# Kernel tuning notes

Hardware: AMD Instinct MI355X
Metric: run time of the kernel (lower is better)

The kernel has to match this reference:

```python
import jax, jax.numpy as jnp
import numpy as np

N = 8000      # nodes
E = 64000     # edges
F = 2560      # in_channels
H = 8         # heads
C = 320       # out_channels per head
G = 16        # graphs in batch
SLOPE = 0.2   # GATv2 default negative_slope


def setup_inputs() -> dict:
    key = jax.random.key(0)
    ks = jax.random.split(key, 20)
    inp = {
        'x': jax.random.normal(ks[0], (N, F), jnp.float32),
        'edge_index': jax.random.randint(ks[1], (2, E), 0, N, dtype=jnp.int64),
        'edge_attr': jax.random.normal(ks[2], (E, 1), jnp.float32),
        'batch': jnp.sort(jax.random.randint(ks[3], (N,), 0, G, dtype=jnp.int64)),
    }
    s_in = 1.0 / np.sqrt(F).astype(np.float32)
    s_att = 1.0 / np.sqrt(C).astype(np.float32)
    k = 4
    for layer in (1, 2):
        inp[f'Wl{layer}'] = jax.random.normal(ks[k + 0], (F, H * C), jnp.float32) * s_in
        inp[f'bl{layer}'] = jnp.zeros((H * C,), jnp.float32)
        inp[f'Wr{layer}'] = jax.random.normal(ks[k + 1], (F, H * C), jnp.float32) * s_in
        inp[f'br{layer}'] = jnp.zeros((H * C,), jnp.float32)
        inp[f'We{layer}'] = jax.random.normal(ks[k + 2], (1, H * C), jnp.float32)
        inp[f'att{layer}'] = jax.random.normal(ks[k + 3], (H, C), jnp.float32) * s_att
        inp[f'bias{layer}'] = jnp.zeros((H * C,), jnp.float32)
        k += 4
    return inp


def gatv2_layer(x, src, dst, edge_attr, Wl, bl, Wr, br, We, att, bias):
    # x: [N,F] -> out: [N, H*C]
    xl = (x @ Wl + bl).reshape(N, H, C)   # source transform (aggregated)
    xr = (x @ Wr + br).reshape(N, H, C)   # target transform
    ee = (edge_attr @ We).reshape(E, H, C)
    m = jax.nn.leaky_relu(xl[src] + xr[dst] + ee, SLOPE)  # [E,H,C]
    score = jnp.einsum('ehc,hc->eh', m, att)               # [E,H]
    # segment softmax over incoming edges of each target node
    smax = jax.ops.segment_max(score, dst, num_segments=N)  # [N,H]
    ex = jnp.exp(score - smax[dst])
    denom = jax.ops.segment_sum(ex, dst, num_segments=N)    # [N,H]
    alpha = ex / denom[dst]                                  # [E,H]
    out = jax.ops.segment_sum(xl[src] * alpha[:, :, None], dst, num_segments=N)
    return out.reshape(N, H * C) + bias


def reference(x, edge_index, edge_attr, batch,
              Wl1, bl1, Wr1, br1, We1, att1, bias1,
              Wl2, bl2, Wr2, br2, We2, att2, bias2):
    src, dst = edge_index[0], edge_index[1]
    h = gatv2_layer(x, src, dst, edge_attr, Wl1, bl1, Wr1, br1, We1, att1, bias1)
    # dropout is identity in eval mode
    h = gatv2_layer(h, src, dst, edge_attr, Wl2, bl2, Wr2, br2, We2, att2, bias2)
    # global mean pool over graphs
    sums = jax.ops.segment_sum(h, batch, num_segments=G)                 # [G, H*C]
    cnt = jax.ops.segment_sum(jnp.ones((N, 1), h.dtype), batch, num_segments=G)
    return sums / jnp.maximum(cnt, 1.0)
```

## Files before the change

kernel.cpp:

```cpp
#include <hip/hip_runtime.h>

typedef unsigned short u16;
typedef _Float16 f16;
typedef _Float16 f16x8 __attribute__((ext_vector_type(8)));
typedef _Float16 f16x2 __attribute__((ext_vector_type(2)));
typedef float f32x4 __attribute__((ext_vector_type(4)));

#define AS1 __attribute__((address_space(1)))
#define AS3 __attribute__((address_space(3)))

constexpr int N_NODES = 8000;
constexpr int N_EDGES = 64000;
constexpr int F_IN    = 2560;
constexpr int HEADS   = 8;
constexpr int CPH     = 320;
constexpr int HC      = 2560;
constexpr int NW      = 5120;
constexpr int NGRAPH  = 16;
constexpr float SLOPE = 0.2f;

__global__ __launch_bounds__(256)
void cvt_f32_f16(const float* __restrict__ in, f16* __restrict__ out, int n)
{
  const int i = (blockIdx.x * 256 + threadIdx.x) * 4;
  if (i >= n) return;
  const float4 v = *(const float4*)(in + i);
  f16 o[4] = {(f16)v.x, (f16)v.y, (f16)v.z, (f16)v.w};
  *(ushort4*)(out + i) = *(const ushort4*)o;
}

__global__ __launch_bounds__(256)
void transpose_w(const float* __restrict__ in, f16* __restrict__ out)
{
  __shared__ u16 tile[64][66];
  const int bx = blockIdx.x * 64;
  const int by = blockIdx.y * 64;
  const int tx = threadIdx.x & 63;
  const int ty = threadIdx.x >> 6;
  #pragma unroll
  for (int i = ty; i < 64; i += 4) {
    f16 h = (f16)in[(size_t)(by + i) * HC + bx + tx];
    u16 u; __builtin_memcpy(&u, &h, 2);
    tile[i][tx] = u;
  }
  __syncthreads();
  #pragma unroll
  for (int i = ty; i < 64; i += 4) {
    u16 u = tile[tx][i];
    f16 h; __builtin_memcpy(&h, &u, 2);
    out[(size_t)(bx + i) * F_IN + by + tx] = h;
  }
}

__global__ __launch_bounds__(512, 2)
void gemm_fused(const f16* __restrict__ A, const f16* __restrict__ BT,
                const float* __restrict__ bl, const float* __restrict__ br,
                f16* __restrict__ XL, f16* __restrict__ XR)
{
  __shared__ __align__(16) f16 sm[65536];
  f16* const sA0 = sm;
  f16* const sA1 = sm + 16384;
  f16* const sB0 = sm + 32768;
  f16* const sB1 = sm + 49152;

  const int t    = threadIdx.x;
  const int lane = t & 63;
  const int wave = t >> 6;

  const int bid0 = (int)blockIdx.x;
  const int xcd  = bid0 & 7;
  const int ic   = bid0 >> 3;
  const int m0   = (xcd * 4 + (ic & 3)) * 256;
  const int n0   = (ic >> 2) * 256;

  const int fm = (wave >> 2) * 128;
  const int fn = (wave & 3) * 64;
  const int ml = lane & 15;
  const int lq = lane >> 4;

  auto stageA = [&](f16* D, int half, int kt) {
    const int k0 = kt * 64;
    #pragma unroll
    for (int jj = 0; jj < 2; ++jj) {
      const int s  = jj * 512 + t;
      const int r  = s >> 3;
      const int lc = (s & 7) ^ (r & 7);
      int gr = m0 + half * 128 + r;
      gr = (gr < N_NODES) ? gr : (N_NODES - 1);
      const f16* g = A + (size_t)gr * F_IN + k0 + lc * 8;
      __builtin_amdgcn_global_load_lds((AS1 const void*)g,
                                       (AS3 void*)(D + half * 8192 + s * 8), 16, 0, 0);
    }
  };
  auto stageB = [&](f16* D, int half, int kt) {
    const int k0 = kt * 64;
    #pragma unroll
    for (int jj = 0; jj < 2; ++jj) {
      const int s  = jj * 512 + t;
      const int r  = s >> 3;
      const int lc = (s & 7) ^ (r & 7);
      const f16* g = BT + (size_t)(n0 + half * 128 + r) * F_IN + k0 + lc * 8;
      __builtin_amdgcn_global_load_lds((AS1 const void*)g,
                                       (AS3 void*)(D + half * 8192 + s * 8), 16, 0, 0);
    }
  };
  auto ldA = [&](const f16* S, int i, int kk) -> f16x8 {
    const int row = fm + i * 16 + ml;
    const int p   = (kk * 4 + lq) ^ (row & 7);
    return *(const f16x8*)(S + row * 64 + p * 8);
  };
  auto ldB = [&](const f16* S, int j, int kk) -> f16x8 {
    const int row = fn + j * 16 + ml;
    const int p   = (kk * 4 + lq) ^ (row & 7);
    return *(const f16x8*)(S + row * 64 + p * 8);
  };

  f32x4 acc[8][4] = {};
  f16x8 bf[4][2];

#define MMROW(i, A0_, A1_)                                                                   \
    _Pragma("unroll")                                                                        \
    for (int j = 0; j < 4; ++j) {                                                            \
      acc[i][j] = __builtin_amdgcn_mfma_f32_16x16x32_f16(A0_, bf[j][0], acc[i][j], 0, 0, 0); \
      acc[i][j] = __builtin_amdgcn_mfma_f32_16x16x32_f16(A1_, bf[j][1], acc[i][j], 0, 0, 0); \
    }

#define PHASE(SA, q, STG)                          \
  {                                                \
    const f16x8 p00 = ldA(SA, 2*(q),     0);       \
    const f16x8 p01 = ldA(SA, 2*(q),     1);       \
    const f16x8 p10 = ldA(SA, 2*(q) + 1, 0);       \
    const f16x8 p11 = ldA(SA, 2*(q) + 1, 1);       \
    STG;                                           \
    __builtin_amdgcn_s_barrier();                  \
    __builtin_amdgcn_sched_barrier(0);             \
    __builtin_amdgcn_s_setprio(1);                 \
    MMROW(2*(q),     p00, p01)                     \
    MMROW(2*(q) + 1, p10, p11)                     \
    __builtin_amdgcn_s_setprio(0);                 \
  }

#define ENDPH() { __builtin_amdgcn_s_barrier(); __builtin_amdgcn_sched_barrier(0); }
#define LOADB(SB) { _Pragma("unroll") for (int j = 0; j < 4; ++j) { bf[j][0] = ldB(SB, j, 0); bf[j][1] = ldB(SB, j, 1); } }

  stageA(sA0, 0, 0); stageA(sA0, 1, 0);
  stageB(sB0, 0, 0); stageB(sB0, 1, 0);
  stageB(sB1, 0, 1); stageB(sB1, 1, 1);
  asm volatile("s_waitcnt vmcnt(4)" ::: "memory");
  __builtin_amdgcn_s_barrier();
  __builtin_amdgcn_sched_barrier(0);

  for (int it = 0; it < 20; ++it) {
    const int T  = 2 * it;
    const int t1 = T + 1;
    const int t2 = (T + 2 < 40) ? T + 2 : 39;
    const int t3 = (T + 3 < 40) ? T + 3 : 39;

    LOADB(sB0)
    PHASE(sA0, 0, stageA(sA1, 0, t1)) ENDPH()
    PHASE(sA0, 1, stageA(sA1, 1, t1)) ENDPH()
    PHASE(sA0, 2, stageB(sB0, 0, t2)) ENDPH()
    PHASE(sA0, 3, stageB(sB0, 1, t2))
    asm volatile("s_waitcnt vmcnt(4)" ::: "memory");
    ENDPH()
    LOADB(sB1)
    PHASE(sA1, 0, stageA(sA0, 0, t2)) ENDPH()
    PHASE(sA1, 1, stageA(sA0, 1, t2)) ENDPH()
    PHASE(sA1, 2, stageB(sB1, 0, t3)) ENDPH()
    PHASE(sA1, 3, stageB(sB1, 1, t3))
    asm volatile("s_waitcnt vmcnt(4)" ::: "memory");
    ENDPH()
  }

#undef MMROW
#undef PHASE
#undef ENDPH
#undef LOADB

  asm volatile("s_waitcnt vmcnt(0)" ::: "memory");
  __builtin_amdgcn_s_barrier();

  const bool left = (n0 < HC);
  f16* __restrict__ OUT = left ? XL : XR;
  const float* __restrict__ bias = left ? bl : br;
  const int nb = left ? n0 : (n0 - HC);
  const int rg = (lane >> 4) * 4;
  f16* const wbase = sm + wave * 8192;

  #pragma unroll
  for (int j = 0; j < 4; ++j) {
    const float bv = bias[nb + fn + j * 16 + ml];
    #pragma unroll
    for (int i = 0; i < 8; ++i) {
      #pragma unroll
      for (int r = 0; r < 4; ++r) {
        const int row = i * 16 + rg + r;
        const int col = j * 16 + ml;
        const int pc  = (col >> 3) ^ (row & 7);
        wbase[row * 64 + pc * 8 + (col & 7)] = (f16)(acc[i][j][r] + bv);
      }
    }
  }
  __syncthreads();
  #pragma unroll
  for (int it = 0; it < 16; ++it) {
    const int row = it * 8 + (lane >> 3);
    const int ch  = lane & 7;
    const int pc  = ch ^ (row & 7);
    const f16x8 v = *(const f16x8*)(wbase + row * 64 + pc * 8);
    const int gm = m0 + fm + row;
    if (gm < N_NODES)
      *(f16x8*)(OUT + (size_t)gm * HC + nb + fn + ch * 8) = v;
  }
}

__global__ __launch_bounds__(256)
void count_edges(const int* __restrict__ dst, int* __restrict__ counts)
{
  const int e = blockIdx.x * 256 + threadIdx.x;
  if (e < N_EDGES) atomicAdd(&counts[dst[e]], 1);
}

__global__ __launch_bounds__(256)
void scan_offsets(const int* __restrict__ counts, int* __restrict__ offs, int* __restrict__ cur)
{
  __shared__ int wtot[4];
  const int t = threadIdx.x;
  const int lane = t & 63, wave = t >> 6;
  const int base = t * 32;
  int loc[32];
  int run = 0;
  #pragma unroll
  for (int i = 0; i < 32; ++i) {
    const int idx = base + i;
    const int v = (idx < N_NODES) ? counts[idx] : 0;
    loc[i] = run;
    run += v;
  }
  int incl = run;
  #pragma unroll
  for (int off = 1; off < 64; off <<= 1) {
    int y = __shfl_up(incl, off, 64);
    if (lane >= off) incl += y;
  }
  const int excl = incl - run;
  if (lane == 63) wtot[wave] = incl;
  __syncthreads();
  int wb = 0;
  for (int wv = 0; wv < wave; ++wv) wb += wtot[wv];
  const int mybase = wb + excl;
  #pragma unroll
  for (int i = 0; i < 32; ++i) {
    const int idx = base + i;
    if (idx < N_NODES) { offs[idx] = mybase + loc[i]; cur[idx] = mybase + loc[i]; }
  }
  if (t == 255) offs[N_NODES] = wb + incl;
}

__global__ __launch_bounds__(256)
void fill_csr(const int* __restrict__ dst, int* __restrict__ cur, int* __restrict__ eids)
{
  const int e = blockIdx.x * 256 + threadIdx.x;
  if (e < N_EDGES) {
    const int p = atomicAdd(&cur[dst[e]], 1);
    eids[p] = e;
  }
}

__global__ __launch_bounds__(256)
void gat_edge_fused(const f16* __restrict__ XL, const f16* __restrict__ XR,
                    const float* __restrict__ We, const float* __restrict__ att,
                    const float* __restrict__ eattr,
                    const int* __restrict__ src,
                    const int* __restrict__ offs, const int* __restrict__ eids,
                    const float* __restrict__ bias,
                    f16* __restrict__ out)
{
  const int n    = blockIdx.x;
  const int t    = threadIdx.x;
  const int wave = t >> 6;
  const int lane = t & 63;
  const int half = lane >> 5;
  const int l32  = lane & 31;
  const int h    = wave * 2 + half;
  const int c8   = h * CPH + l32 * 8;
  const int c2   = h * CPH + 256 + l32 * 2;

  float xr[10], wv[10], av[10];
  {
    const f16x8 v8 = *(const f16x8*)(XR + (size_t)n * HC + c8);
    const f16x2 v2 = *(const f16x2*)(XR + (size_t)n * HC + c2);
    #pragma unroll
    for (int k = 0; k < 8; ++k) xr[k] = (float)v8[k];
    xr[8] = (float)v2[0]; xr[9] = (float)v2[1];
  }
  {
    const float4 w0 = *(const float4*)(We + c8);
    const float4 w1 = *(const float4*)(We + c8 + 4);
    const float4 a0 = *(const float4*)(att + c8);
    const float4 a1 = *(const float4*)(att + c8 + 4);
    wv[0]=w0.x; wv[1]=w0.y; wv[2]=w0.z; wv[3]=w0.w;
    wv[4]=w1.x; wv[5]=w1.y; wv[6]=w1.z; wv[7]=w1.w;
    av[0]=a0.x; av[1]=a0.y; av[2]=a0.z; av[3]=a0.w;
    av[4]=a1.x; av[5]=a1.y; av[6]=a1.z; av[7]=a1.w;
    wv[8] = We[c2]; wv[9] = We[c2 + 1];
    av[8] = att[c2]; av[9] = att[c2 + 1];
  }

  float m = -3.0e38f, l = 0.f;
  float acc[10];
  #pragma unroll
  for (int k = 0; k < 10; ++k) acc[k] = 0.f;

  const int b = offs[n], e = offs[n + 1];
  if (b < e) {
    int eidA = eids[b];
    int sA   = src[eidA];
    float eaA = eattr[eidA];
    f16x8 v8A = *(const f16x8*)(XL + (size_t)sA * HC + c8);
    f16x2 v2A = *(const f16x2*)(XL + (size_t)sA * HC + c2);
    int sB; float eaB;
    if (b + 1 < e) { const int eid = eids[b + 1]; sB = src[eid]; eaB = eattr[eid]; }
    else           { sB = sA; eaB = 0.f; }

    for (int p = b; p < e; ++p) {
      const f16* rowN = XL + (size_t)sB * HC;
      const f16x8 v8N = *(const f16x8*)(rowN + c8);
      const f16x2 v2N = *(const f16x2*)(rowN + c2);
      const int pn   = (p + 2 < e) ? (p + 2) : (e - 1);
      const int eidN = eids[pn];
      const int sC   = src[eidN];
      const float eaC = eattr[eidN];

      float xl[10];
      #pragma unroll
      for (int k = 0; k < 8; ++k) xl[k] = (float)v8A[k];
      xl[8] = (float)v2A[0]; xl[9] = (float)v2A[1];
      float partial = 0.f;
      #pragma unroll
      for (int k = 0; k < 10; ++k) {
        float v = xl[k] + xr[k] + eaA * wv[k];
        v = (v > 0.f) ? v : SLOPE * v;
        partial += v * av[k];
      }
      #pragma unroll
      for (int msk = 16; msk >= 1; msk >>= 1)
        partial += __shfl_xor(partial, msk, 64);
      const float sc    = partial;
      const float mn    = fmaxf(m, sc);
      const float scale = __expf(m - mn);
      const float w     = __expf(sc - mn);
      l = l * scale + w;
      #pragma unroll
      for (int k = 0; k < 10; ++k) acc[k] = acc[k] * scale + w * xl[k];
      m = mn;

      v8A = v8N; v2A = v2N; eaA = eaB;
      sB = sC; eaB = eaC;
    }
  }

  const float inv = (l > 0.f) ? 1.f / l : 0.f;
  f16x8 s8;
  #pragma unroll
  for (int k = 0; k < 8; ++k) s8[k] = (f16)(acc[k] * inv + bias[c8 + k]);
  f16x2 s2;
  s2[0] = (f16)(acc[8] * inv + bias[c2]);
  s2[1] = (f16)(acc[9] * inv + bias[c2 + 1]);
  *(f16x8*)(out + (size_t)n * HC + c8) = s8;
  *(f16x2*)(out + (size_t)n * HC + c2) = s2;
}

__global__ __launch_bounds__(256)
void pool_kernel(const f16* __restrict__ Hm, const int* __restrict__ batch, float* __restrict__ out)
{
  __shared__ int se[2];
  const int g = blockIdx.x;
  const int chunk = blockIdx.y;
  const int t = threadIdx.x;
  if (t < 2) {
    const int target = g + t;
    int lo = 0, hi = N_NODES;
    while (lo < hi) { const int mid = (lo + hi) >> 1; if (batch[mid] < target) lo = mid + 1; else hi = mid; }
    se[t] = lo;
  }
  __syncthreads();
  const int s0 = se[0], s1 = se[1];
  const int c = chunk * 256 + t;
  float sum = 0.f;
  for (int n = s0; n < s1; ++n) sum += (float)Hm[(size_t)n * HC + c];
  int cnt = s1 - s0; if (cnt < 1) cnt = 1;
  out[g * HC + c] = sum / (float)cnt;
}

static void run_layer(const f16* A, const float* Wl, const float* bl,
                      const float* Wr, const float* br,
                      const float* We, const float* att, const float* bias,
                      const int* src, const float* eattr,
                      f16* WT, f16* XL, f16* XR,
                      const int* offs, const int* eids, f16* OUT, hipStream_t stream)
{
  dim3 tgrid(HC / 64, F_IN / 64);
  transpose_w<<<tgrid, 256, 0, stream>>>(Wl, WT);
  transpose_w<<<tgrid, 256, 0, stream>>>(Wr, WT + (size_t)HC * F_IN);
  gemm_fused<<<32 * (NW / 256), 512, 0, stream>>>(A, WT, bl, br, XL, XR);
  gat_edge_fused<<<N_NODES, 256, 0, stream>>>(XL, XR, We, att, eattr, src, offs, eids, bias, OUT);
}

extern "C" void kernel_launch(void* const* d_in, const int* in_sizes, int n_in,
                              void* d_out, int out_size, void* d_ws, size_t ws_size,
                              hipStream_t stream)
{
  const float* x     = (const float*)d_in[0];
  const int*   eidx  = (const int*)d_in[1];
  const float* eattr = (const float*)d_in[2];
  const int*   batch = (const int*)d_in[3];
  const float* Wl1  = (const float*)d_in[4];
  const float* bl1  = (const float*)d_in[5];
  const float* Wr1  = (const float*)d_in[6];
  const float* br1  = (const float*)d_in[7];
  const float* We1  = (const float*)d_in[8];
  const float* att1 = (const float*)d_in[9];
  const float* bias1= (const float*)d_in[10];
  const float* Wl2  = (const float*)d_in[11];
  const float* bl2  = (const float*)d_in[12];
  const float* Wr2  = (const float*)d_in[13];
  const float* br2  = (const float*)d_in[14];
  const float* We2  = (const float*)d_in[15];
  const float* att2 = (const float*)d_in[16];
  const float* bias2= (const float*)d_in[17];
  float* out = (float*)d_out;

  const int* src = eidx;
  const int* dst = eidx + N_EDGES;

  char* w = (char*)d_ws;
  auto take = [&](size_t b) { char* p = w; w += (b + 255) & ~(size_t)255; return p; };
  f16*   Xh    = (f16*)take((size_t)N_NODES * F_IN * 2);
  f16*   H2h   = (f16*)take((size_t)N_NODES * HC * 2);
  f16*   WT    = (f16*)take((size_t)NW * F_IN * 2);
  f16*   XL    = (f16*)take((size_t)N_NODES * HC * 2);
  f16*   XR    = (f16*)take((size_t)N_NODES * HC * 2);
  int*   counts= (int*)take((size_t)N_NODES * 4);
  int*   offs  = (int*)take((size_t)(N_NODES + 1) * 4);
  int*   cur   = (int*)take((size_t)N_NODES * 4);
  int*   eids  = (int*)take((size_t)N_EDGES * 4);

  hipMemsetAsync(counts, 0, N_NODES * 4, stream);
  count_edges<<<N_EDGES / 256, 256, 0, stream>>>(dst, counts);
  scan_offsets<<<1, 256, 0, stream>>>(counts, offs, cur);
  fill_csr<<<N_EDGES / 256, 256, 0, stream>>>(dst, cur, eids);

  cvt_f32_f16<<<(N_NODES * F_IN) / 1024, 256, 0, stream>>>(x, Xh, N_NODES * F_IN);

  run_layer(Xh, Wl1, bl1, Wr1, br1, We1, att1, bias1, src, eattr,
            WT, XL, XR, offs, eids, Xh, stream);
  run_layer(Xh, Wl2, bl2, Wr2, br2, We2, att2, bias2, src, eattr,
            WT, XL, XR, offs, eids, H2h, stream);

  pool_kernel<<<dim3(NGRAPH, HC / 256), 256, 0, stream>>>(H2h, batch, out);
}
```

Measured before the change: 915.4 us.

## Pack edge src/attr into CSR and process edge pairs with deeper prefetch

The CSR fill now stores each edge's source index and edge attribute as one int2, so the edge kernel no longer chases the index through eids to src and eattr. The aggregation loop handles two edges per step, merging their scores into the online softmax together, and prefetches row data four edges ahead. The goal is to hide gather latency and cut the dependent loads per edge. The cost is more registers per thread, which may lower occupancy, and extra tail handling for nodes with an odd number of incoming edges.

New measurement: 936.9 us. 2.3% more time.

```diff
diff --git a/kernel.cpp b/kernel.cpp
--- a/kernel.cpp
+++ b/kernel.cpp
@@ -258,21 +258,21 @@
 }
 
 __global__ __launch_bounds__(256)
-void fill_csr(const int* __restrict__ dst, int* __restrict__ cur, int* __restrict__ eids)
+void fill_csr(const int* __restrict__ dst, const int* __restrict__ srcv,
+              const float* __restrict__ ea, int* __restrict__ cur,
+              int2* __restrict__ ecsr)
 {
   const int e = blockIdx.x * 256 + threadIdx.x;
   if (e < N_EDGES) {
     const int p = atomicAdd(&cur[dst[e]], 1);
-    eids[p] = e;
+    ecsr[p] = make_int2(srcv[e], __float_as_int(ea[e]));
   }
 }
 
 __global__ __launch_bounds__(256)
 void gat_edge_fused(const f16* __restrict__ XL, const f16* __restrict__ XR,
                     const float* __restrict__ We, const float* __restrict__ att,
-                    const float* __restrict__ eattr,
-                    const int* __restrict__ src,
-                    const int* __restrict__ offs, const int* __restrict__ eids,
+                    const int2* __restrict__ ecsr, const int* __restrict__ offs,
                     const float* __restrict__ bias,
                     f16* __restrict__ out)
 {
@@ -313,51 +313,81 @@
   for (int k = 0; k < 10; ++k) acc[k] = 0.f;
 
   const int b = offs[n], e = offs[n + 1];
-  if (b < e) {
-    int eidA = eids[b];
-    int sA   = src[eidA];
-    float eaA = eattr[eidA];
-    f16x8 v8A = *(const f16x8*)(XL + (size_t)sA * HC + c8);
-    f16x2 v2A = *(const f16x2*)(XL + (size_t)sA * HC + c2);
-    int sB; float eaB;
-    if (b + 1 < e) { const int eid = eids[b + 1]; sB = src[eid]; eaB = eattr[eid]; }
-    else           { sB = sA; eaB = 0.f; }
-
-    for (int p = b; p < e; ++p) {
-      const f16* rowN = XL + (size_t)sB * HC;
-      const f16x8 v8N = *(const f16x8*)(rowN + c8);
-      const f16x2 v2N = *(const f16x2*)(rowN + c2);
-      const int pn   = (p + 2 < e) ? (p + 2) : (e - 1);
-      const int eidN = eids[pn];
-      const int sC   = src[eidN];
-      const float eaC = eattr[eidN];
-
-      float xl[10];
+  const int d = e - b;
+  if (d > 0) {
+    const int np = (d + 1) >> 1;
+
+    auto ldmeta = [&](int pi, int2* mm) {
+      pi = (pi < np) ? pi : (np - 1);
+      const int q0 = b + 2 * pi;
+      const int q1 = q0 + 1;
+      mm[0] = ecsr[q0];
+      mm[1] = ecsr[(q1 < e) ? q1 : q0];
+    };
+    auto ldrows = [&](const int2* mm, f16x8* v8, f16x2* v2) {
+      const f16* r0 = XL + (size_t)mm[0].x * HC;
+      const f16* r1 = XL + (size_t)mm[1].x * HC;
+      v8[0] = *(const f16x8*)(r0 + c8);
+      v8[1] = *(const f16x8*)(r1 + c8);
+      v2[0] = *(const f16x2*)(r0 + c2);
+      v2[1] = *(const f16x2*)(r1 + c2);
+    };
+    auto compute_pair = [&](const f16x8* V8, const f16x2* V2, const int2* M, int i) {
+      const bool v1 = (b + 2 * i + 1) < e;
+      const float ea0 = __int_as_float(M[0].y);
+      const float ea1 = __int_as_float(M[1].y);
+      float xl0[10], xl1[10];
       #pragma unroll
-      for (int k = 0; k < 8; ++k) xl[k] = (float)v8A[k];
-      xl[8] = (float)v2A[0]; xl[9] = (float)v2A[1];
-      float partial = 0.f;
+      for (int k = 0; k < 8; ++k) { xl0[k] = (float)V8[0][k]; xl1[k] = (float)V8[1][k]; }
+      xl0[8] = (float)V2[0][0]; xl0[9] = (float)V2[0][1];
+      xl1[8] = (float)V2[1][0]; xl1[9] = (float)V2[1][1];
+      float p0 = 0.f, p1 = 0.f;
       #pragma unroll
       for (int k = 0; k < 10; ++k) {
-        float v = xl[k] + xr[k] + eaA * wv[k];
-        v = (v > 0.f) ? v : SLOPE * v;
-        partial += v * av[k];
+        float a0 = xl0[k] + xr[k] + ea0 * wv[k];
+        float a1 = xl1[k] + xr[k] + ea1 * wv[k];
+        a0 = (a0 > 0.f) ? a0 : SLOPE * a0;
+        a1 = (a1 > 0.f) ? a1 : SLOPE * a1;
+        p0 += a0 * av[k];
+        p1 += a1 * av[k];
       }
       #pragma unroll
-      for (int msk = 16; msk >= 1; msk >>= 1)
-        partial += __shfl_xor(partial, msk, 64);
-      const float sc    = partial;
-      const float mn    = fmaxf(m, sc);
+      for (int msk = 16; msk >= 1; msk >>= 1) {
+        p0 += __shfl_xor(p0, msk, 64);
+        p1 += __shfl_xor(p1, msk, 64);
+      }
+      const float s1v   = v1 ? p1 : -3.0e38f;
+      const float mn    = fmaxf(m, fmaxf(p0, s1v));
       const float scale = __expf(m - mn);
-      const float w     = __expf(sc - mn);
-      l = l * scale + w;
+      const float w0    = __expf(p0 - mn);
+      const float w1    = __expf(s1v - mn);
+      l = l * scale + w0 + w1;
       #pragma unroll
-      for (int k = 0; k < 10; ++k) acc[k] = acc[k] * scale + w * xl[k];
+      for (int k = 0; k < 10; ++k) acc[k] = acc[k] * scale + w0 * xl0[k] + w1 * xl1[k];
       m = mn;
-
-      v8A = v8N; v2A = v2N; eaA = eaB;
-      sB = sC; eaB = eaC;
+    };
+
+    int2 mA[2], mB[2], mC[2], mD[2];
+    f16x8 A8[2], B8[2], C8r[2], D8r[2];
+    f16x2 A2[2], B2[2], C2r[2], D2r[2];
+    ldmeta(0, mA); ldmeta(1, mB);
+    ldrows(mA, A8, A2);
+    ldrows(mB, B8, B2);
+    ldmeta(2, mC); ldmeta(3, mD);
+
+    int i = 0;
+    for (; i + 1 < np; i += 2) {
+      ldrows(mC, C8r, C2r);
+      compute_pair(A8, A2, mA, i);
+      ldrows(mD, D8r, D2r);
+      compute_pair(B8, B2, mB, i + 1);
+      mA[0] = mC[0]; mA[1] = mC[1];
+      mB[0] = mD[0]; mB[1] = mD[1];
+      ldmeta(i + 4, mC); ldmeta(i + 5, mD);
+      A8[0] = C8r[0]; A8[1] = C8r[1]; A2[0] = C2r[0]; A2[1] = C2r[1];
+      B8[0] = D8r[0]; B8[1] = D8r[1]; B2[0] = D2r[0]; B2[1] = D2r[1];
     }
+    if (i < np) compute_pair(A8, A2, mA, i);
   }
 
   const float inv = (l > 0.f) ? 1.f / l : 0.f;
@@ -396,15 +426,14 @@
 static void run_layer(const f16* A, const float* Wl, const float* bl,
                       const float* Wr, const float* br,
                       const float* We, const float* att, const float* bias,
-                      const int* src, const float* eattr,
                       f16* WT, f16* XL, f16* XR,
-                      const int* offs, const int* eids, f16* OUT, hipStream_t stream)
+                      const int* offs, const int2* ecsr, f16* OUT, hipStream_t stream)
 {
   dim3 tgrid(HC / 64, F_IN / 64);
   transpose_w<<<tgrid, 256, 0, stream>>>(Wl, WT);
   transpose_w<<<tgrid, 256, 0, stream>>>(Wr, WT + (size_t)HC * F_IN);
   gemm_fused<<<32 * (NW / 256), 512, 0, stream>>>(A, WT, bl, br, XL, XR);
-  gat_edge_fused<<<N_NODES, 256, 0, stream>>>(XL, XR, We, att, eattr, src, offs, eids, bias, OUT);
+  gat_edge_fused<<<N_NODES, 256, 0, stream>>>(XL, XR, We, att, ecsr, offs, bias, OUT);
 }
 
 extern "C" void kernel_launch(void* const* d_in, const int* in_sizes, int n_in,
@@ -444,19 +473,19 @@
   int*   counts= (int*)take((size_t)N_NODES * 4);
   int*   offs  = (int*)take((size_t)(N_NODES + 1) * 4);
   int*   cur   = (int*)take((size_t)N_NODES * 4);
-  int*   eids  = (int*)take((size_t)N_EDGES * 4);
+  int2*  ecsr  = (int2*)take((size_t)N_EDGES * 8);
 
   hipMemsetAsync(counts, 0, N_NODES * 4, stream);
   count_edges<<<N_EDGES / 256, 256, 0, stream>>>(dst, counts);
   scan_offsets<<<1, 256, 0, stream>>>(counts, offs, cur);
-  fill_csr<<<N_EDGES / 256, 256, 0, stream>>>(dst, cur, eids);
+  fill_csr<<<N_EDGES / 256, 256, 0, stream>>>(dst, src, eattr, cur, ecsr);
 
   cvt_f32_f16<<<(N_NODES * F_IN) / 1024, 256, 0, stream>>>(x, Xh, N_NODES * F_IN);
 
-  run_layer(Xh, Wl1, bl1, Wr1, br1, We1, att1, bias1, src, eattr,
-            WT, XL, XR, offs, eids, Xh, stream);
-  run_layer(Xh, Wl2, bl2, Wr2, br2, We2, att2, bias2, src, eattr,
-            WT, XL, XR, offs, eids, H2h, stream);
+  run_layer(Xh, Wl1, bl1, Wr1, br1, We1, att1, bias1,
+            WT, XL, XR, offs, ecsr, Xh, stream);
+  run_layer(Xh, Wl2, bl2, Wr2, br2, We2, att2, bias2,
+            WT, XL, XR, offs, ecsr, H2h, stream);
 
   pool_kernel<<<dim3(NGRAPH, HC / 256), 256, 0, stream>>>(H2h, batch, out);
 }
```
